# Kernel optimization log

Measured on AMD Instinct MI355X. Metric: run time of the kernel, lower is better.

The kernel has to match this reference:

```python
import jax, jax.numpy as jnp
import numpy as np

NEG_BIG = -9.0e15  # mask value from original code (-9000000000000000.0)


def setup_inputs() -> dict:
    key = jax.random.key(0)
    k1, k2, k3, k4, k5 = jax.random.split(key, 5)
    B, N, M, D = 32, 1024, 1024, 128
    input1 = jax.random.normal(k1, (B, N, D), dtype=jnp.float32)
    input2 = jax.random.normal(k2, (B, M, D), dtype=jnp.float32)
    adj = jax.random.randint(k3, (B, N, M), 0, 2, dtype=jnp.int32)
    # xavier_normal on (D,1): std = gain*sqrt(2/(fan_in+fan_out)) = 1.414*sqrt(2/(D+1))
    std = 1.414 * np.sqrt(2.0 / (D + 1))
    a1 = jax.random.normal(k4, (D, 1), dtype=jnp.float32) * std
    a2 = jax.random.normal(k5, (D, 1), dtype=jnp.float32) * std
    return {"input1": input1, "input2": input2, "adj": adj, "a1": a1, "a2": a2}


def reference(input1, input2, adj, a1, a2):
    h, g = input1, input2
    # e1: (B,N,1), e2: (B,1,M); broadcast add replaces the repeat() calls
    e1 = jnp.matmul(h, a1)                      # (B,N,1)
    e2 = jnp.matmul(g, a2).transpose(0, 2, 1)   # (B,1,M)
    e = jax.nn.leaky_relu(e1 + e2, negative_slope=0.2)  # (B,N,M)
    attention = jnp.where(adj > 0, e, NEG_BIG)
    attention = jax.nn.softmax(attention, axis=2)
    attention = jnp.where(jnp.isnan(attention), 0.0, attention)
    # per-batch loop in original builds adj_[b,i,j] = adj[b,i,:].sum(); vectorized:
    deg = jnp.sum(adj, axis=2, keepdims=True).astype(attention.dtype)  # (B,N,1)
    attention = attention * deg
    h_prime = jnp.matmul(attention, g)          # (B,N,D)
    return h_prime
```

## Files before the change

### kernel.cpp

```cpp
#include <hip/hip_runtime.h>

#define BB 32
#define NN 1024
#define MM 1024
#define DD 128

typedef __attribute__((ext_vector_type(4))) float f32x4;
typedef __attribute__((ext_vector_type(8))) __bf16 bf16x8;
typedef unsigned short ushort_t;
typedef unsigned int uint_t;

#define L2E 1.44269504f
#define KEXP 9.357623e-14f
#define KEXPINV 1.0686475e13f

__device__ __forceinline__ unsigned f2bf(float x) {
    unsigned u = __builtin_bit_cast(unsigned, x);
    return (u + 0x7fffu + ((u >> 16) & 1u)) >> 16;
}

#define GLOAD16(gp, lp)                                                     \
    __builtin_amdgcn_global_load_lds(                                       \
        (const __attribute__((address_space(1))) unsigned int*)(gp),        \
        (__attribute__((address_space(3))) unsigned int*)(lp), 16, 0, 0)

__global__ __launch_bounds__(256) void prep(
    const float* __restrict__ g, const float* __restrict__ h,
    const float* __restrict__ a1, const float* __restrict__ a2,
    ushort_t* __restrict__ gq, float* __restrict__ e1, float* __restrict__ e2)
{
    __shared__ ushort_t tl[DD][66];
    int b = blockIdx.y, m0 = blockIdx.x * 64, t = threadIdx.x;

    #pragma unroll
    for (int i = 0; i < 8; i++) {
        int idx = i * 256 + t;
        int m = idx >> 5;
        int c4 = (idx & 31) * 4;
        float4 v = *(const float4*)(h + ((size_t)(b * NN + m0 + m)) * DD + c4);
        float4 av = *(const float4*)(a1 + c4);
        float p = v.x * av.x + v.y * av.y + v.z * av.z + v.w * av.w;
        #pragma unroll
        for (int s = 16; s; s >>= 1) p += __shfl_xor(p, s);
        if ((t & 31) == 0) e1[b * NN + m0 + m] = p;
    }
    #pragma unroll
    for (int i = 0; i < 8; i++) {
        int idx = i * 256 + t;
        int m = idx >> 5;
        int c4 = (idx & 31) * 4;
        float4 v = *(const float4*)(g + ((size_t)(b * MM + m0 + m)) * DD + c4);
        tl[c4 + 0][m] = (ushort_t)f2bf(v.x);
        tl[c4 + 1][m] = (ushort_t)f2bf(v.y);
        tl[c4 + 2][m] = (ushort_t)f2bf(v.z);
        tl[c4 + 3][m] = (ushort_t)f2bf(v.w);
        float4 av = *(const float4*)(a2 + c4);
        float p = v.x * av.x + v.y * av.y + v.z * av.z + v.w * av.w;
        #pragma unroll
        for (int s = 16; s; s >>= 1) p += __shfl_xor(p, s);
        if ((t & 31) == 0) e2[b * MM + m0 + m] = p;
    }
    __syncthreads();
    #pragma unroll
    for (int i = 0; i < 4; i++) {
        int idx = i * 256 + t;
        int d = idx >> 3;
        int c = (idx & 7) * 8;
        int4 o;
        o.x = (int)((unsigned)tl[d][c + 0] | ((unsigned)tl[d][c + 1] << 16));
        o.y = (int)((unsigned)tl[d][c + 2] | ((unsigned)tl[d][c + 3] << 16));
        o.z = (int)((unsigned)tl[d][c + 4] | ((unsigned)tl[d][c + 5] << 16));
        o.w = (int)((unsigned)tl[d][c + 6] | ((unsigned)tl[d][c + 7] << 16));
        int mg = m0 + c;
        *(int4*)(gq + (((size_t)((b * 32 + (mg >> 5)) * DD + d)) << 5) + (mg & 31)) = o;
    }
}

__global__ __launch_bounds__(256, 2) void attn_tiled(
    const int* __restrict__ adj, const ushort_t* __restrict__ gq,
    const float* __restrict__ e1, const float* __restrict__ e2,
    float* __restrict__ out)
{
    __shared__ __align__(16) float e2S[MM];
    __shared__ __align__(16) int adjS[4][64 * 32];
    __shared__ __align__(16) ushort_t gqS[4][128 * 32];

    int b = blockIdx.y, n0 = blockIdx.x * 64, t = threadIdx.x;
    int wid = t >> 6, lane = t & 63;
    int rlo = lane & 15, hh = lane >> 4;
    int r = wid * 16 + rlo;
    int r8 = r & 7;

    {
        float4 ev = *(const float4*)(e2 + b * MM + t * 4);
        ev.x *= L2E; ev.y *= L2E; ev.z *= L2E; ev.w *= L2E;
        *(float4*)(&e2S[t * 4]) = ev;
    }
    float e1f = L2E * e1[b * NN + n0 + r];
    __syncthreads();

    const int* adjb = adj + (size_t)(b * NN + n0) * MM;
    const ushort_t* gqb = gq + (size_t)b * (32 * DD * 32);

    int adi0 = t, adi1 = t + 256;
    int arow0 = adi0 >> 3, aseg0 = (adi0 & 7) ^ (arow0 & 7);
    int arow1 = adi1 >> 3, aseg1 = (adi1 & 7) ^ (arow1 & 7);
    int gd0 = adi0 >> 2, gseg0 = (adi0 & 3) ^ ((gd0 >> 1) & 3);
    int gd1 = adi1 >> 2, gseg1 = (adi1 & 3) ^ ((gd1 >> 1) & 3);

#define STAGE(P, K) do {                                                    \
        GLOAD16(adjb + (size_t)arow0 * MM + (K) * 32 + aseg0 * 4,           \
                &adjS[P][adi0 * 4]);                                        \
        GLOAD16(adjb + (size_t)arow1 * MM + (K) * 32 + aseg1 * 4,           \
                &adjS[P][adi1 * 4]);                                        \
        GLOAD16(gqb + (size_t)(K) * 4096 + gd0 * 32 + gseg0 * 8,            \
                &gqS[P][adi0 * 8]);                                         \
        GLOAD16(gqb + (size_t)(K) * 4096 + gd1 * 32 + gseg1 * 8,            \
                &gqS[P][adi1 * 8]);                                         \
    } while (0)

    f32x4 acc[8];
    #pragma unroll
    for (int j = 0; j < 8; j++) acc[j] = (f32x4){0.f, 0.f, 0.f, 0.f};
    float zl = 0.f, dl = 0.f;

#define COMPUTE(P, K) do {                                                  \
        int4 a0 = *(const int4*)(&adjS[P][r * 32 + ((2 * hh) ^ r8) * 4]);   \
        int4 a1 = *(const int4*)(&adjS[P][r * 32 + ((2 * hh + 1) ^ r8) * 4]);\
        float4 ev0 = *(const float4*)(&e2S[(K) * 32 + 8 * hh]);             \
        float4 ev1 = *(const float4*)(&e2S[(K) * 32 + 8 * hh + 4]);         \
        float ex[8] = {ev0.x, ev0.y, ev0.z, ev0.w,                          \
                       ev1.x, ev1.y, ev1.z, ev1.w};                         \
        int   ax[8] = {a0.x, a0.y, a0.z, a0.w, a1.x, a1.y, a1.z, a1.w};     \
        bf16x8 af;                                                          \
        _Pragma("unroll")                                                   \
        for (int jj = 0; jj < 8; jj++) {                                    \
            float sp = e1f + ex[jj];                                        \
            float lk = fmaxf(sp, 0.2f * sp);                                \
            float sel = (ax[jj] > 0) ? KEXP : 0.f;                          \
            float wv = sel * __builtin_amdgcn_exp2f(lk);                    \
            zl += wv;                                                       \
            dl += sel;                                                      \
            af[jj] = (__bf16)wv;                                            \
        }                                                                   \
        _Pragma("unroll")                                                   \
        for (int j = 0; j < 8; j++) {                                       \
            int d = j * 16 + rlo;                                           \
            int4 bv = *(const int4*)(                                       \
                &gqS[P][d * 32 + (hh ^ ((rlo >> 1) & 3)) * 8]);             \
            acc[j] = __builtin_amdgcn_mfma_f32_16x16x32_bf16(               \
                         af, __builtin_bit_cast(bf16x8, bv), acc[j], 0,0,0);\
        }                                                                   \
    } while (0)

    STAGE(0, 0); STAGE(1, 1); STAGE(2, 2);

    for (int k = 0; k < 30; ++k) {
        asm volatile("s_waitcnt vmcnt(8)" ::: "memory");
        __builtin_amdgcn_s_barrier();
        __builtin_amdgcn_sched_barrier(0);
        if (k < 29) STAGE((k + 3) & 3, k + 3);
        COMPUTE(k & 3, k);
    }
    asm volatile("s_waitcnt vmcnt(4)" ::: "memory");
    __builtin_amdgcn_s_barrier();
    __builtin_amdgcn_sched_barrier(0);
    COMPUTE(2, 30);
    asm volatile("s_waitcnt vmcnt(0)" ::: "memory");
    __builtin_amdgcn_s_barrier();
    __builtin_amdgcn_sched_barrier(0);
    COMPUTE(3, 31);

#undef COMPUTE
#undef STAGE

    zl += __shfl_xor(zl, 16); zl += __shfl_xor(zl, 32);
    dl += __shfl_xor(dl, 16); dl += __shfl_xor(dl, 32);
    float sc = (dl > 0.f) ? (dl * KEXPINV) / zl : 0.f;

    float scr[4];
    #pragma unroll
    for (int rg = 0; rg < 4; rg++) scr[rg] = __shfl(sc, 4 * hh + rg);

    float* ob = out + ((size_t)(b * NN + n0 + wid * 16)) * DD + rlo;
    #pragma unroll
    for (int j = 0; j < 8; j++)
        #pragma unroll
        for (int rg = 0; rg < 4; rg++)
            ob[(size_t)(4 * hh + rg) * DD + j * 16] = acc[j][rg] * scr[rg];
}

extern "C" void kernel_launch(void* const* d_in, const int* in_sizes, int n_in,
                              void* d_out, int out_size, void* d_ws, size_t ws_size,
                              hipStream_t stream) {
    const float* h   = (const float*)d_in[0];
    const float* g   = (const float*)d_in[1];
    const int*   adj = (const int*)d_in[2];
    const float* a1  = (const float*)d_in[3];
    const float* a2  = (const float*)d_in[4];
    float* out = (float*)d_out;

    char* ws = (char*)d_ws;
    float*    e1 = (float*)(ws);
    float*    e2 = (float*)(ws + (128u << 10));
    ushort_t* gq = (ushort_t*)(ws + (512u << 10));

    prep<<<dim3(MM / 64, BB), 256, 0, stream>>>(g, h, a1, a2, gq, e1, e2);
    attn_tiled<<<dim3(NN / 64, BB), 256, 0, stream>>>(adj, gq, e1, e2, out);
}
```

Baseline: 48.09 us.

## Factor exp of leaky-relu into per-row and per-column exponentials, split waves 2x2

Factors exp(leaky_relu(e1+e2)) into products of per-row and per-column exponentials. The column factors for both slopes are precomputed in prep and packed as two bf16 values, so the inner loop does a compare and a multiply instead of an exp per element. It also reorganises the four waves into a 2x2 grid of row-halves and D-halves, so each wave computes two row fragments against half the columns and reuses its gq B-fragments across both. The column exponentials are stored in bf16 and the constant softmax shift is dropped, which risks overflow or underflow for large logits and costs precision.

```diff
diff --git a/kernel.cpp b/kernel.cpp
--- a/kernel.cpp
+++ b/kernel.cpp
@@ -11,12 +11,16 @@
 typedef unsigned int uint_t;
 
 #define L2E 1.44269504f
-#define KEXP 9.357623e-14f
-#define KEXPINV 1.0686475e13f
 
 __device__ __forceinline__ unsigned f2bf(float x) {
     unsigned u = __builtin_bit_cast(unsigned, x);
     return (u + 0x7fffu + ((u >> 16) & 1u)) >> 16;
+}
+__device__ __forceinline__ float bflo(uint_t u) {
+    return __builtin_bit_cast(float, u << 16);
+}
+__device__ __forceinline__ float bfhi(uint_t u) {
+    return __builtin_bit_cast(float, u & 0xffff0000u);
 }
 
 #define GLOAD16(gp, lp)                                                     \
@@ -27,7 +31,8 @@
 __global__ __launch_bounds__(256) void prep(
     const float* __restrict__ g, const float* __restrict__ h,
     const float* __restrict__ a1, const float* __restrict__ a2,
-    ushort_t* __restrict__ gq, float* __restrict__ e1, float* __restrict__ e2)
+    ushort_t* __restrict__ gq, float* __restrict__ e1,
+    uint_t* __restrict__ BD)
 {
     __shared__ ushort_t tl[DD][66];
     int b = blockIdx.y, m0 = blockIdx.x * 64, t = threadIdx.x;
@@ -58,7 +63,11 @@
         float p = v.x * av.x + v.y * av.y + v.z * av.z + v.w * av.w;
         #pragma unroll
         for (int s = 16; s; s >>= 1) p += __shfl_xor(p, s);
-        if ((t & 31) == 0) e2[b * MM + m0 + m] = p;
+        if ((t & 31) == 0) {
+            uint_t pb = f2bf(__builtin_amdgcn_exp2f(L2E * p));
+            uint_t pd = f2bf(__builtin_amdgcn_exp2f(0.2f * L2E * p));
+            BD[b * MM + m0 + m] = pb | (pd << 16);
+        }
     }
     __syncthreads();
     #pragma unroll
@@ -78,25 +87,27 @@
 
 __global__ __launch_bounds__(256, 2) void attn_tiled(
     const int* __restrict__ adj, const ushort_t* __restrict__ gq,
-    const float* __restrict__ e1, const float* __restrict__ e2,
+    const float* __restrict__ e1, const uint_t* __restrict__ BD,
     float* __restrict__ out)
 {
-    __shared__ __align__(16) float e2S[MM];
+    __shared__ __align__(16) uint_t BDS[MM];
     __shared__ __align__(16) int adjS[4][64 * 32];
     __shared__ __align__(16) ushort_t gqS[4][128 * 32];
 
     int b = blockIdx.y, n0 = blockIdx.x * 64, t = threadIdx.x;
     int wid = t >> 6, lane = t & 63;
+    int wr = wid >> 1, wd = wid & 1;
     int rlo = lane & 15, hh = lane >> 4;
-    int r = wid * 16 + rlo;
-    int r8 = r & 7;
-
-    {
-        float4 ev = *(const float4*)(e2 + b * MM + t * 4);
-        ev.x *= L2E; ev.y *= L2E; ev.z *= L2E; ev.w *= L2E;
-        *(float4*)(&e2S[t * 4]) = ev;
-    }
-    float e1f = L2E * e1[b * NN + n0 + r];
+
+    *(uint4*)(&BDS[t * 4]) = *(const uint4*)(BD + b * MM + t * 4);
+    float An[2], Cn[2], invA[2];
+    #pragma unroll
+    for (int f = 0; f < 2; f++) {
+        float e1r = e1[b * NN + n0 + wr * 32 + f * 16 + rlo];
+        An[f]   = __builtin_amdgcn_exp2f(L2E * e1r);
+        Cn[f]   = __builtin_amdgcn_exp2f(0.2f * L2E * e1r);
+        invA[f] = __builtin_amdgcn_exp2f(-L2E * e1r);
+    }
     __syncthreads();
 
     const int* adjb = adj + (size_t)(b * NN + n0) * MM;
@@ -119,37 +130,50 @@
                 &gqS[P][adi1 * 8]);                                         \
     } while (0)
 
-    f32x4 acc[8];
-    #pragma unroll
-    for (int j = 0; j < 8; j++) acc[j] = (f32x4){0.f, 0.f, 0.f, 0.f};
-    float zl = 0.f, dl = 0.f;
+    f32x4 acc[2][4];
+    #pragma unroll
+    for (int f = 0; f < 2; f++)
+        #pragma unroll
+        for (int j = 0; j < 4; j++) acc[f][j] = (f32x4){0.f, 0.f, 0.f, 0.f};
+    float zl[2] = {0.f, 0.f};
+    int dcnt[2] = {0, 0};
 
 #define COMPUTE(P, K) do {                                                  \
-        int4 a0 = *(const int4*)(&adjS[P][r * 32 + ((2 * hh) ^ r8) * 4]);   \
-        int4 a1 = *(const int4*)(&adjS[P][r * 32 + ((2 * hh + 1) ^ r8) * 4]);\
-        float4 ev0 = *(const float4*)(&e2S[(K) * 32 + 8 * hh]);             \
-        float4 ev1 = *(const float4*)(&e2S[(K) * 32 + 8 * hh + 4]);         \
-        float ex[8] = {ev0.x, ev0.y, ev0.z, ev0.w,                          \
-                       ev1.x, ev1.y, ev1.z, ev1.w};                         \
-        int   ax[8] = {a0.x, a0.y, a0.z, a0.w, a1.x, a1.y, a1.z, a1.w};     \
-        bf16x8 af;                                                          \
+        uint4 bd0 = *(const uint4*)(&BDS[(K) * 32 + 8 * hh]);               \
+        uint4 bd1 = *(const uint4*)(&BDS[(K) * 32 + 8 * hh + 4]);           \
+        uint_t bdv[8] = {bd0.x, bd0.y, bd0.z, bd0.w,                        \
+                         bd1.x, bd1.y, bd1.z, bd1.w};                       \
+        int4 cb[4];                                                         \
         _Pragma("unroll")                                                   \
-        for (int jj = 0; jj < 8; jj++) {                                    \
-            float sp = e1f + ex[jj];                                        \
-            float lk = fmaxf(sp, 0.2f * sp);                                \
-            float sel = (ax[jj] > 0) ? KEXP : 0.f;                          \
-            float wv = sel * __builtin_amdgcn_exp2f(lk);                    \
-            zl += wv;                                                       \
-            dl += sel;                                                      \
-            af[jj] = (__bf16)wv;                                            \
+        for (int j = 0; j < 4; j++) {                                       \
+            int d = wd * 64 + j * 16 + rlo;                                 \
+            cb[j] = *(const int4*)(                                         \
+                &gqS[P][d * 32 + (hh ^ ((rlo >> 1) & 3)) * 8]);             \
         }                                                                   \
         _Pragma("unroll")                                                   \
-        for (int j = 0; j < 8; j++) {                                       \
-            int d = j * 16 + rlo;                                           \
-            int4 bv = *(const int4*)(                                       \
-                &gqS[P][d * 32 + (hh ^ ((rlo >> 1) & 3)) * 8]);             \
-            acc[j] = __builtin_amdgcn_mfma_f32_16x16x32_bf16(               \
-                         af, __builtin_bit_cast(bf16x8, bv), acc[j], 0,0,0);\
+        for (int f = 0; f < 2; f++) {                                       \
+            int r = wr * 32 + f * 16 + rlo;                                 \
+            int r8 = r & 7;                                                 \
+            int4 a0 = *(const int4*)(                                       \
+                &adjS[P][r * 32 + ((2 * hh) ^ r8) * 4]);                    \
+            int4 a1 = *(const int4*)(                                       \
+                &adjS[P][r * 32 + ((2 * hh + 1) ^ r8) * 4]);                \
+            int ax[8] = {a0.x, a0.y, a0.z, a0.w, a1.x, a1.y, a1.z, a1.w};   \
+            bf16x8 af;                                                      \
+            _Pragma("unroll")                                               \
+            for (int jj = 0; jj < 8; jj++) {                                \
+                float Bv = bflo(bdv[jj]);                                   \
+                float Dv = bfhi(bdv[jj]);                                   \
+                float val = (Bv > invA[f]) ? Bv * An[f] : Dv * Cn[f];       \
+                float wv = (ax[jj] > 0) ? val : 0.f;                        \
+                zl[f] += wv;                                                \
+                dcnt[f] += ax[jj];                                          \
+                af[jj] = (__bf16)wv;                                        \
+            }                                                               \
+            _Pragma("unroll")                                               \
+            for (int j = 0; j < 4; j++)                                     \
+                acc[f][j] = __builtin_amdgcn_mfma_f32_16x16x32_bf16(        \
+                    af, __builtin_bit_cast(bf16x8, cb[j]), acc[f][j], 0,0,0);\
         }                                                                   \
     } while (0)
 
@@ -174,20 +198,25 @@
 #undef COMPUTE
 #undef STAGE
 
-    zl += __shfl_xor(zl, 16); zl += __shfl_xor(zl, 32);
-    dl += __shfl_xor(dl, 16); dl += __shfl_xor(dl, 32);
-    float sc = (dl > 0.f) ? (dl * KEXPINV) / zl : 0.f;
-
-    float scr[4];
-    #pragma unroll
-    for (int rg = 0; rg < 4; rg++) scr[rg] = __shfl(sc, 4 * hh + rg);
-
-    float* ob = out + ((size_t)(b * NN + n0 + wid * 16)) * DD + rlo;
-    #pragma unroll
-    for (int j = 0; j < 8; j++)
-        #pragma unroll
-        for (int rg = 0; rg < 4; rg++)
-            ob[(size_t)(4 * hh + rg) * DD + j * 16] = acc[j][rg] * scr[rg];
+    #pragma unroll
+    for (int f = 0; f < 2; f++) {
+        zl[f] += __shfl_xor(zl[f], 16); zl[f] += __shfl_xor(zl[f], 32);
+        dcnt[f] += __shfl_xor(dcnt[f], 16); dcnt[f] += __shfl_xor(dcnt[f], 32);
+    }
+
+    float* ob = out + ((size_t)(b * NN + n0 + wr * 32)) * DD + wd * 64 + rlo;
+    #pragma unroll
+    for (int f = 0; f < 2; f++) {
+        float sc = (dcnt[f] > 0) ? ((float)dcnt[f] / zl[f]) : 0.f;
+        #pragma unroll
+        for (int rg = 0; rg < 4; rg++) {
+            float scv = __shfl(sc, 4 * hh + rg);
+            #pragma unroll
+            for (int j = 0; j < 4; j++)
+                ob[(size_t)(f * 16 + 4 * hh + rg) * DD + j * 16] =
+                    acc[f][j][rg] * scv;
+        }
+    }
 }
 
 extern "C" void kernel_launch(void* const* d_in, const int* in_sizes, int n_in,
@@ -202,9 +231,9 @@
 
     char* ws = (char*)d_ws;
     float*    e1 = (float*)(ws);
-    float*    e2 = (float*)(ws + (128u << 10));
+    uint_t*   BD = (uint_t*)(ws + (128u << 10));
     ushort_t* gq = (ushort_t*)(ws + (512u << 10));
 
-    prep<<<dim3(MM / 64, BB), 256, 0, stream>>>(g, h, a1, a2, gq, e1, e2);
-    attn_tiled<<<dim3(NN / 64, BB), 256, 0, stream>>>(adj, gq, e1, e2, out);
-}
+    prep<<<dim3(MM / 64, BB), 256, 0, stream>>>(g, h, a1, a2, gq, e1, BD);
+    attn_tiled<<<dim3(NN / 64, BB), 256, 0, stream>>>(adj, gq, e1, BD, out);
+}
```

Result: slower. 52.88 us (+10.0%).
